# Optimization experiments

Hardware: AMD Instinct MI355X
Metric: run time of the kernel (lower is better)

Reference implementation:

```python
import jax, jax.numpy as jnp
import numpy as np

RE_PER_PRB = 12  # resource elements (subcarriers) per PRB in 5G NR


def _forward(y, h_hat_ls, dmrs_ofdm_pos, dmrs_subcarrier_pos):
    S = y.shape[2]  # num_ofdm_symbols (y used for its shape only)
    # [B, num_pilots, T, R] -> [B, R, T, num_pilots]
    h = jnp.transpose(h_hat_ls, (0, 3, 2, 1))
    B, R, T, P = h.shape
    # FOCC removal: average adjacent pilot pairs, duplicate back (sum/2, repeat 2)
    h = h.reshape(B, R, T, P // 2, 2).sum(axis=-1, keepdims=True) * 0.5
    h = jnp.broadcast_to(h, (B, R, T, P // 2, 2)).reshape(B, R, T, P)

    npd = dmrs_subcarrier_pos.shape[1]   # pilots per DMRS symbol per PRB
    nds = dmrs_ofdm_pos.shape[-1]        # number of DMRS OFDM symbols
    nprb = P // (npd * nds)              # number of PRBs
    RE = RE_PER_PRB

    # --- nearest-pilot indices + positional encodings, per tx (as in torch code,
    # torch.meshgrid default indexing='ij') ---
    re_pos = jnp.stack(
        jnp.meshgrid(jnp.arange(RE), jnp.arange(S), indexing='ij'), axis=-1
    ).reshape(-1, 1, 2)  # [RE*S, 1, 2]

    def per_tx(sc_pos, of_pos):
        pil = jnp.stack(jnp.meshgrid(sc_pos, of_pos, indexing='ij'), axis=-1).reshape(1, -1, 2)
        diff = jnp.abs(re_pos - pil)                  # [RE*S, npd*nds, 2] Manhattan components
        nn = jnp.argmin(diff.sum(-1), axis=1).reshape(S, RE)
        pe = diff.min(axis=1).reshape(S, RE, 2).transpose(1, 0, 2).astype(jnp.float32)  # [RE, S, 2]
        norm = lambda x: (x - x.mean()) / (x.std(ddof=1) + 1e-8)  # torch .std() is unbiased
        # channel order swapped exactly as in the torch code: [time-dist, freq-dist]
        return nn, jnp.stack([norm(pe[..., 1]), norm(pe[..., 0])], axis=-1)

    nn_idx, pe = jax.vmap(per_tx)(dmrs_subcarrier_pos, dmrs_ofdm_pos)  # [T,S,RE], [T,RE,S,2]
    pe = jnp.tile(pe, (1, nprb, 1, 1))  # [T, nprb*RE, S, 2]

    # --- group pilots per PRB ---
    # pilot layout in h_hat_ls: (dmrs_symbol, prb, subcarrier); per-PRB pilot index
    # = subcarrier*nds + symbol to match the meshgrid('ij') flattening above
    hp = h.reshape(B, R, T, nds, nprb, npd).transpose(0, 1, 2, 4, 5, 3)
    hp = hp.reshape(B, R, T, nprb, npd * nds)  # [B,R,T,nprb,pilots_per_prb]

    # --- nearest-neighbor gather onto the full resource grid ---
    gather_tx = lambda hp_t, nn_t: hp_t[..., nn_t]  # [B,R,nprb,Np] , [S,RE] -> [B,R,nprb,S,RE]
    gathered = jax.vmap(gather_tx, in_axes=(2, 0), out_axes=2)(hp, nn_idx)  # [B,R,T,nprb,S,RE]

    # -> [B, T, num_subcarriers, S, R]
    h_full = gathered.transpose(0, 2, 3, 5, 4, 1).reshape(B, T, nprb * RE, S, R)
    return h_full, pe


def setup_inputs() -> dict:
    key = jax.random.key(0)
    k1, k2 = jax.random.split(key)
    B, R, T, S = 16, 16, 4, 14
    nprb, npd, nds = 273, 6, 2
    P = nds * nprb * npd  # 3276 pilots
    y = jax.random.normal(k1, (B, R, S, nprb * RE_PER_PRB), dtype=jnp.float32)
    h_hat_ls = jax.random.normal(k2, (B, P, T, R), dtype=jnp.float32)
    dmrs_ofdm_pos = jnp.broadcast_to(jnp.array([2, 11], dtype=jnp.int32), (T, nds))
    dmrs_subcarrier_pos = jnp.broadcast_to(jnp.arange(0, 12, 2, dtype=jnp.int32), (T, npd))
    return {"y": y, "h_hat_ls": h_hat_ls, "dmrs_ofdm_pos": dmrs_ofdm_pos,
            "dmrs_subcarrier_pos": dmrs_subcarrier_pos}


def reference(y, h_hat_ls, dmrs_ofdm_pos, dmrs_subcarrier_pos):
    return _forward(y, h_hat_ls, dmrs_ofdm_pos, dmrs_subcarrier_pos)
```

## Files before the change

### kernel.cpp

```cpp
#include <hip/hip_runtime.h>

#define B_   16
#define R_   16
#define T_   4
#define S_   14
#define NPRB 273
#define NPD  6
#define NDS  2
#define RE_  12
#define P_   (NDS*NPRB*NPD)
#define NSC  (NPRB*RE_)
#define F_   (RE_*S_)

#define NH   (B_*T_*NSC*S_*R_)
#define NPE  (T_*NSC*S_*2)
#define NH4  (NH/4)
#define NPE4 (NPE/4)

#define CHUNK4   (RE_*S_*R_/4)
#define NBLK_PE  ((NPE4 + 255)/256)
#define NBLK_H   (B_*T_*NPRB)

typedef float f4 __attribute__((ext_vector_type(4)));

__global__ __launch_bounds__(256) void fused_kernel(
    const float* __restrict__ hls,
    const int* __restrict__ ofdm_pos,
    const int* __restrict__ sc_pos,
    float* __restrict__ out)
{
    const int bid = blockIdx.x;
    const int tid = threadIdx.x;

    if (bid >= NBLK_PE) {
        __shared__ int perm_sh[F_];
        __shared__ f4  avg_sh[6*4];

        const int hb  = bid - NBLK_PE;
        const int prb = hb % NPRB;
        const int bt  = hb / NPRB;
        const int t   = bt & (T_-1);

        if (tid < F_) {
            const int v  = tid;
            const int kl = v / S_, s = v - (v / S_)*S_;
            const int jp = s*RE_ + kl;
            const int rej = jp / S_, sj = jp - (jp / S_)*S_;
            int best = 1 << 30, bestj = 0;
            for (int sci = 0; sci < NPD; ++sci) {
                const int dsc = abs(rej - sc_pos[t*NPD + sci]);
                for (int ofi = 0; ofi < NDS; ++ofi) {
                    const int dof = abs(sj - ofdm_pos[t*NDS + ofi]);
                    const int d = dsc + dof;
                    if (d < best) { best = d; bestj = sci*NDS + ofi; }
                }
            }
            perm_sh[v] = (bestj & 1)*3 + (bestj >> 2);
        } else if (tid >= 192 && tid < 216) {
            const int j    = tid - 192;
            const int code = j >> 2, r4 = j & 3;
            const int ds   = (code >= 3) ? 1 : 0;
            const int scp  = code - 3*ds;
            const int b    = bt >> 2;
            const int p0   = ds*(NPRB*NPD) + prb*NPD + 2*scp;
            const f4* src = (const f4*)hls + ((b*P_ + p0)*T_ + t)*4 + r4;
            const f4 a = src[0];
            const f4 c = src[T_*4];
            avg_sh[j] = 0.5f*(a + c);
        }
        __syncthreads();

        f4* out4 = (f4*)out + (size_t)bt*(NSC*S_*R_/4) + (size_t)prb*CHUNK4;
        #pragma unroll
        for (int u = tid; u < CHUNK4; u += 256) {
            const int r4 = u & 3;
            const int v  = u >> 2;
            const int code = perm_sh[v];
            __builtin_nontemporal_store(avg_sh[code*4 + r4], &out4[u]);
        }
    } else {
        __shared__ float dt_sh[T_*F_];
        __shared__ float df_sh[T_*F_];
        __shared__ float stats[T_][4];

        for (int e = tid; e < T_*F_; e += 256) {
            const int t  = e / F_, j = e - (e / F_)*F_;
            const int rej = j / S_, sj = j - (j / S_)*S_;
            int dfmin = 1 << 30, dtmin = 1 << 30;
            for (int sci = 0; sci < NPD; ++sci) {
                const int dsc = abs(rej - sc_pos[t*NPD + sci]);
                if (dsc < dfmin) dfmin = dsc;
            }
            for (int ofi = 0; ofi < NDS; ++ofi) {
                const int dof = abs(sj - ofdm_pos[t*NDS + ofi]);
                if (dof < dtmin) dtmin = dof;
            }
            dt_sh[e] = (float)dtmin;
            df_sh[e] = (float)dfmin;
        }
        __syncthreads();

        const int w = tid >> 6, lane = tid & 63;
        {
            float sdt = 0.f, sdf = 0.f;
            for (int j = lane; j < F_; j += 64) { sdt += dt_sh[w*F_+j]; sdf += df_sh[w*F_+j]; }
            for (int o = 32; o > 0; o >>= 1) { sdt += __shfl_down(sdt, o); sdf += __shfl_down(sdf, o); }
            if (lane == 0) { stats[w][0] = sdt/(float)F_; stats[w][2] = sdf/(float)F_; }
        }
        __syncthreads();
        {
            const float mt = stats[w][0], mf = stats[w][2];
            float vt = 0.f, vf = 0.f;
            for (int j = lane; j < F_; j += 64) {
                const float a = dt_sh[w*F_+j] - mt; vt += a*a;
                const float b = df_sh[w*F_+j] - mf; vf += b*b;
            }
            for (int o = 32; o > 0; o >>= 1) { vt += __shfl_down(vt, o); vf += __shfl_down(vf, o); }
            if (lane == 0) {
                stats[w][1] = 1.0f/(sqrtf(vt/(float)(F_-1)) + 1e-8f);
                stats[w][3] = 1.0f/(sqrtf(vf/(float)(F_-1)) + 1e-8f);
            }
        }
        __syncthreads();

        const int q = bid*256 + tid;
        if (q < NPE4) {
            const int g0 = q*4;
            float vv[4];
            #pragma unroll
            for (int u2 = 0; u2 < 4; ++u2) {
                const int g  = g0 + u2;
                const int c  = g & 1;
                const int g1 = g >> 1;
                const int s  = g1 % S_;
                const int g2 = g1 / S_;
                const int i  = g2 % NSC;
                const int t  = g2 / NSC;
                const int re = i % RE_;
                const int j  = s*RE_ + re;
                const float d = (c == 0) ? dt_sh[t*F_ + j] : df_sh[t*F_ + j];
                vv[u2] = (d - stats[t][2*c]) * stats[t][2*c + 1];
            }
            f4 o; o.x = vv[0]; o.y = vv[1]; o.z = vv[2]; o.w = vv[3];
            __builtin_nontemporal_store(o, (f4*)(out + NH) + q);
        }
    }
}

extern "C" void kernel_launch(void* const* d_in, const int* in_sizes, int n_in,
                              void* d_out, int out_size, void* d_ws, size_t ws_size,
                              hipStream_t stream) {
    const float* hls  = (const float*)d_in[1];
    const int*   ofdm = (const int*)d_in[2];
    const int*   scp  = (const int*)d_in[3];
    float* out = (float*)d_out;

    hipLaunchKernelGGL(fused_kernel, dim3(NBLK_PE + NBLK_H), dim3(256), 0, stream,
                       hls, ofdm, scp, out);
}
```

Baseline: 223.4 us.

## Process 13 PRBs per block with double-buffered pilot averages

Each block now handles 13 consecutive PRBs instead of one, so the nearest-pilot permutation is computed once per block and the block count drops 13x. Pilot loads for the next PRB are issued before the current PRB's stores, and the averages are double-buffered in shared memory so the loads overlap the store loop. The averages are padded to a stride of 5 to avoid bank conflicts. The cost is a barrier per PRB and less parallelism, with 1344 write blocks.

New measurement: 232.5 us. 1.04x slower.

```diff
diff --git a/kernel.cpp b/kernel.cpp
--- a/kernel.cpp
+++ b/kernel.cpp
@@ -18,8 +18,10 @@
 #define NPE4 (NPE/4)
 
 #define CHUNK4   (RE_*S_*R_/4)
+#define PRB_PER_BLK 13
+#define NGRP        21
 #define NBLK_PE  ((NPE4 + 255)/256)
-#define NBLK_H   (B_*T_*NPRB)
+#define NBLK_H   (B_*T_*NGRP)
 
 typedef float f4 __attribute__((ext_vector_type(4)));
 
@@ -34,14 +36,29 @@
 
     if (bid >= NBLK_PE) {
         __shared__ int perm_sh[F_];
-        __shared__ f4  avg_sh[6*4];
+        __shared__ f4  avg_sh[2][6*5];
 
         const int hb  = bid - NBLK_PE;
-        const int prb = hb % NPRB;
-        const int bt  = hb / NPRB;
+        const int grp = hb % NGRP;
+        const int bt  = hb / NGRP;
         const int t   = bt & (T_-1);
+        const int b   = bt >> 2;
+        const int prb0 = grp * PRB_PER_BLK;
 
-        if (tid < F_) {
+        const bool loader = (tid >= 192 && tid < 216);
+        const int  j    = tid - 192;
+        const int  code = j >> 2, r4 = j & 3;
+        const int  ds   = (code >= 3) ? 1 : 0;
+        const int  scp  = code - 3*ds;
+        const f4* base = (const f4*)hls
+                       + ((size_t)(b*P_ + ds*(NPRB*NPD) + 2*scp)*T_ + t)*4 + r4;
+
+        f4 a, c;
+        if (loader) {
+            const f4* s = base + (size_t)prb0 * 96;
+            a = s[0];
+            c = s[16];
+        } else if (tid < F_) {
             const int v  = tid;
             const int kl = v / S_, s = v - (v / S_)*S_;
             const int jp = s*RE_ + kl;
@@ -55,28 +72,29 @@
                     if (d < best) { best = d; bestj = sci*NDS + ofi; }
                 }
             }
-            perm_sh[v] = (bestj & 1)*3 + (bestj >> 2);
-        } else if (tid >= 192 && tid < 216) {
-            const int j    = tid - 192;
-            const int code = j >> 2, r4 = j & 3;
-            const int ds   = (code >= 3) ? 1 : 0;
-            const int scp  = code - 3*ds;
-            const int b    = bt >> 2;
-            const int p0   = ds*(NPRB*NPD) + prb*NPD + 2*scp;
-            const f4* src = (const f4*)hls + ((b*P_ + p0)*T_ + t)*4 + r4;
-            const f4 a = src[0];
-            const f4 c = src[T_*4];
-            avg_sh[j] = 0.5f*(a + c);
+            perm_sh[v] = ((bestj & 1)*3 + (bestj >> 2)) * 5;
         }
+        if (loader) avg_sh[0][code*5 + r4] = 0.5f*(a + c);
         __syncthreads();
 
-        f4* out4 = (f4*)out + (size_t)bt*(NSC*S_*R_/4) + (size_t)prb*CHUNK4;
-        #pragma unroll
-        for (int u = tid; u < CHUNK4; u += 256) {
-            const int r4 = u & 3;
-            const int v  = u >> 2;
-            const int code = perm_sh[v];
-            __builtin_nontemporal_store(avg_sh[code*4 + r4], &out4[u]);
+        f4* outb = (f4*)out + (size_t)bt*(NSC*S_*R_/4) + (size_t)prb0*CHUNK4;
+        for (int i = 0; i < PRB_PER_BLK; ++i) {
+            if (loader && (i+1 < PRB_PER_BLK)) {
+                const f4* s = base + (size_t)(prb0 + i + 1) * 96;
+                a = s[0];
+                c = s[16];
+            }
+            const int bufi = i & 1;
+            f4* outp = outb + (size_t)i * CHUNK4;
+            for (int u = tid; u < CHUNK4; u += 256) {
+                const int r4s = u & 3;
+                const int v   = u >> 2;
+                __builtin_nontemporal_store(avg_sh[bufi][perm_sh[v] + r4s],
+                                            &outp[u]);
+            }
+            if (loader && (i+1 < PRB_PER_BLK))
+                avg_sh[bufi ^ 1][code*5 + r4] = 0.5f*(a + c);
+            __syncthreads();
         }
     } else {
         __shared__ float dt_sh[T_*F_];
```

## Process two PRB instances per wavefront, four wavefronts per block

Applied to the files above, without the earlier changes.

Restructures the broadcast-write part so each 256-thread block handles eight (b,t,prb) instances, with each 64-lane wavefront writing two adjacent PRB chunks through one contiguous 21-iteration store loop. Nearest-pilot permutations are precomputed for all four tx in shared memory, and the averaged pilots are laid out with stride 5 to reduce bank conflicts. This cuts block count and per-block setup overhead, and it removes the idle lanes of the old 672-store loop over 256 threads. In exchange, each block now recomputes the permutation table for all T, which adds some redundant work.

Result: slower. 228.4 us (+2.2%).

```diff
diff --git a/kernel.cpp b/kernel.cpp
--- a/kernel.cpp
+++ b/kernel.cpp
@@ -18,8 +18,10 @@
 #define NPE4 (NPE/4)
 
 #define CHUNK4   (RE_*S_*R_/4)
+#define NINST    (B_*T_*NPRB)
+#define NPAIR    (NINST/2)
 #define NBLK_PE  ((NPE4 + 255)/256)
-#define NBLK_H   (B_*T_*NPRB)
+#define NBLK_H   (NPAIR/4)
 
 typedef float f4 __attribute__((ext_vector_type(4)));
 
@@ -33,50 +35,61 @@
     const int tid = threadIdx.x;
 
     if (bid >= NBLK_PE) {
-        __shared__ int perm_sh[F_];
-        __shared__ f4  avg_sh[6*4];
+        __shared__ int perm_sh[T_][F_];
+        __shared__ f4  avg_sh[4][60];
 
-        const int hb  = bid - NBLK_PE;
-        const int prb = hb % NPRB;
-        const int bt  = hb / NPRB;
-        const int t   = bt & (T_-1);
+        const int hb   = bid - NBLK_PE;
+        const int w    = tid >> 6, lane = tid & 63;
+        const int inst0 = (hb*4 + w) * 2;
 
-        if (tid < F_) {
-            const int v  = tid;
+        for (int e = tid; e < T_*F_; e += 256) {
+            const int tt = e / F_;
+            const int v  = e - tt*F_;
             const int kl = v / S_, s = v - (v / S_)*S_;
             const int jp = s*RE_ + kl;
             const int rej = jp / S_, sj = jp - (jp / S_)*S_;
             int best = 1 << 30, bestj = 0;
             for (int sci = 0; sci < NPD; ++sci) {
-                const int dsc = abs(rej - sc_pos[t*NPD + sci]);
+                const int dsc = abs(rej - sc_pos[tt*NPD + sci]);
                 for (int ofi = 0; ofi < NDS; ++ofi) {
-                    const int dof = abs(sj - ofdm_pos[t*NDS + ofi]);
+                    const int dof = abs(sj - ofdm_pos[tt*NDS + ofi]);
                     const int d = dsc + dof;
                     if (d < best) { best = d; bestj = sci*NDS + ofi; }
                 }
             }
-            perm_sh[v] = (bestj & 1)*3 + (bestj >> 2);
-        } else if (tid >= 192 && tid < 216) {
-            const int j    = tid - 192;
-            const int code = j >> 2, r4 = j & 3;
+            perm_sh[tt][v] = ((bestj & 1)*3 + (bestj >> 2)) * 5;
+        }
+
+        if (lane < 48) {
+            const int pl   = lane >= 24;
+            const int l24  = lane - 24*pl;
+            const int code = l24 >> 2, r4 = l24 & 3;
             const int ds   = (code >= 3) ? 1 : 0;
             const int scp  = code - 3*ds;
+            const int inst = inst0 + pl;
+            const int bt   = inst / NPRB;
+            const int prb  = inst - bt*NPRB;
+            const int t    = bt & (T_-1);
             const int b    = bt >> 2;
             const int p0   = ds*(NPRB*NPD) + prb*NPD + 2*scp;
-            const f4* src = (const f4*)hls + ((b*P_ + p0)*T_ + t)*4 + r4;
+            const f4* src = (const f4*)hls + ((size_t)(b*P_ + p0)*T_ + t)*4 + r4;
             const f4 a = src[0];
-            const f4 c = src[T_*4];
-            avg_sh[j] = 0.5f*(a + c);
+            const f4 c = src[16];
+            avg_sh[w][pl*30 + code*5 + r4] = 0.5f*(a + c);
         }
         __syncthreads();
 
-        f4* out4 = (f4*)out + (size_t)bt*(NSC*S_*R_/4) + (size_t)prb*CHUNK4;
-        #pragma unroll
-        for (int u = tid; u < CHUNK4; u += 256) {
-            const int r4 = u & 3;
-            const int v  = u >> 2;
-            const int code = perm_sh[v];
-            __builtin_nontemporal_store(avg_sh[code*4 + r4], &out4[u]);
+        const int t0 = ( inst0      / NPRB) & (T_-1);
+        const int t1 = ((inst0 + 1) / NPRB) & (T_-1);
+        f4* outp = (f4*)out + (size_t)inst0 * CHUNK4;
+        for (int i = 0; i < 21; ++i) {
+            const int u  = i*64 + lane;
+            const int q  = u >> 2;
+            const int pl = (q >= F_) ? 1 : 0;
+            const int v  = q - F_*pl;
+            const int tt = pl ? t1 : t0;
+            const int idx = pl*30 + perm_sh[tt][v] + (u & 3);
+            __builtin_nontemporal_store(avg_sh[w][idx], &outp[u]);
         }
     } else {
         __shared__ float dt_sh[T_*F_];
```
